# Kernel optimization log

Measured on AMD Instinct MI355X. Metric: run time of the kernel, lower is better.

Reference implementation:

```python
import jax, jax.numpy as jnp
from jax import lax
import numpy as np

TOPK = 100
SCALE = 4.0
EXCEPT_THRESH = 0.01

B, C, H, W = 16, 80, 256, 256


def setup_inputs() -> dict:
    key = jax.random.key(0)
    k1, k2, k3 = jax.random.split(key, 3)
    heatmap = jax.random.uniform(k1, (B, C, H, W), dtype=jnp.float32)
    offset = jax.random.normal(k2, (B, 2, H, W), dtype=jnp.float32)
    wh = jax.random.uniform(k3, (B, 2, H, W), dtype=jnp.float32)
    return {"heatmap": heatmap, "offset": offset, "wh": wh}


def reference(heatmap, offset, wh):
    b, c, h, w = heatmap.shape
    # 3x3 max-pool NMS: keep only local peaks
    pooled = lax.reduce_window(heatmap, -jnp.inf, lax.max,
                               (1, 1, 3, 3), (1, 1, 1, 1), "SAME")
    keep = (pooled == heatmap).astype(heatmap.dtype)
    hm = keep * heatmap
    # top-k over all classes x spatial positions
    flat = hm.reshape(b, -1)                      # [B, C*H*W]
    scores, indices = lax.top_k(flat, TOPK)       # [B, K]
    scores = scores[:, :, None]                   # [B, K, 1]
    ids = (indices // (h * w)).astype(jnp.float32)[:, :, None]
    spatial = indices % (h * w)                   # [B, K] flat spatial index
    topk_ys = (spatial // w).astype(jnp.float32)
    topk_xs = (spatial % w).astype(jnp.float32)
    # gather offset / wh at peak locations
    off = offset.transpose(0, 2, 3, 1).reshape(b, -1, 2)   # [B, H*W, 2]
    whr = wh.transpose(0, 2, 3, 1).reshape(b, -1, 2)       # [B, H*W, 2]
    off_g = jnp.take_along_axis(off, spatial[:, :, None], axis=1)  # [B, K, 2]
    wh_g = jnp.take_along_axis(whr, spatial[:, :, None], axis=1)   # [B, K, 2]
    cx = topk_xs + off_g[:, :, 0]
    cy = topk_ys + off_g[:, :, 1]
    half_w = wh_g[:, :, 0] * 0.5
    half_h = wh_g[:, :, 1] * 0.5
    bboxes = jnp.stack([cx - half_w, cy - half_h, cx + half_w, cy + half_h], axis=-1)  # [B, K, 4]
    # mask out low-score detections with -1
    mask = scores > EXCEPT_THRESH                 # [B, K, 1]
    neg1 = jnp.float32(-1.0)
    ids = jnp.where(mask, ids, neg1)
    scores = jnp.where(mask, scores, neg1)
    bboxes = jnp.where(mask, bboxes, neg1)
    return ids, scores, bboxes * SCALE
```

## Files before the change

kernel.cpp:

```cpp
#include <hip/hip_runtime.h>
#include <stdint.h>

#define HB 16
#define HC 80
#define HH 256
#define HWD 256
#define PLANE (HH * HWD)
#define NPLANES (HB * HC)
#define K_TOP 100
#define CAP 2048
#define CAPR (CAP / 256)
#define OUTCAP 256
#define NEG_INF (-3.402823466e38f)

__device__ __forceinline__ bool better(float a, int ai, float b, int bi) {
    return (a > b) || (a == b && ai < bi);
}

__device__ void bitonic256(float* sv, int* si) {
    int t = threadIdx.x;
    for (unsigned k = 2; k <= 256; k <<= 1) {
        for (unsigned j = k >> 1; j > 0; j >>= 1) {
            __syncthreads();
            unsigned i = (unsigned)t, x = i ^ j;
            if (x > i) {
                float a = sv[i], bv = sv[x];
                int ai = si[i], bi = si[x];
                bool sw = ((i & k) == 0) ? better(bv, bi, a, ai) : better(a, ai, bv, bi);
                if (sw) { sv[i] = bv; si[i] = bi; sv[x] = a; si[x] = ai; }
            }
        }
    }
    __syncthreads();
}

__device__ __forceinline__ float4 loadrow(const float* __restrict__ pl, int r, int lane) {
    int rc = min(max(r, 0), HH - 1);
    float4 v = ((const float4*)(pl + rc * HWD))[lane];
    if (r != rc) { v.x = NEG_INF; v.y = NEG_INF; v.z = NEG_INF; v.w = NEG_INF; }
    return v;
}

__device__ __forceinline__ float4 hmax4(float4 v, int lane) {
    float vl = __shfl_up(v.w, 1);
    float vr = __shfl_down(v.x, 1);
    if (lane == 0) vl = NEG_INF;
    if (lane == 63) vr = NEG_INF;
    float4 h;
    h.x = fmaxf(fmaxf(vl, v.x), v.y);
    h.y = fmaxf(fmaxf(v.x, v.y), v.z);
    h.z = fmaxf(fmaxf(v.y, v.z), v.w);
    h.w = fmaxf(fmaxf(v.z, v.w), vr);
    return h;
}

__global__ __launch_bounds__(256, 4) void k_plane_topk(const float* __restrict__ heat,
                                                       float* __restrict__ wsv,
                                                       int* __restrict__ wsi) {
    int plane = blockIdx.x;
    int c = plane % HC;
    const float* pl = heat + (size_t)plane * PLANE;
    int t = threadIdx.x;
    int lane = t & 63;
    int wid = t >> 6;
    int rs = wid << 6;

    __shared__ float bufv[CAP];
    __shared__ int   bufi[CAP];
    __shared__ float outv[OUTCAP];
    __shared__ int   outi[OUTCAP];
    __shared__ int   cnt, cnt2;
    __shared__ int   sred8[8];
    __shared__ float smax4[4];

    float thr = 0.99f;
    int n = 0;
    for (int attempt = 0; attempt < 3; ++attempt) {
        if (t == 0) cnt = 0;
        __syncthreads();

        float4 rm1 = loadrow(pl, rs - 1, lane);
        float4 r0  = loadrow(pl, rs, lane);
        float4 g0 = loadrow(pl, rs + 1, lane);
        float4 g1 = loadrow(pl, rs + 2, lane);
        float4 g2 = loadrow(pl, rs + 3, lane);
        float4 g3 = loadrow(pl, rs + 4, lane);
        float4 hA = hmax4(rm1, lane);
        float4 hB = hmax4(r0, lane);
        float4 vB = r0;
        int colb = lane << 2;

        for (int i = 0; i < 64; i += 4) {
            float4 m0 = loadrow(pl, rs + i + 5, lane);
            float4 m1 = loadrow(pl, rs + i + 6, lane);
            float4 m2 = loadrow(pl, rs + i + 7, lane);
            float4 m3 = loadrow(pl, rs + i + 8, lane);
#pragma unroll
            for (int u = 0; u < 4; ++u) {
                float4 nr = (u == 0) ? g0 : (u == 1) ? g1 : (u == 2) ? g2 : g3;
                int row = rs + i + u;
                float4 hC = hmax4(nr, lane);
                float p0 = fmaxf(fmaxf(hA.x, hB.x), hC.x);
                float p1 = fmaxf(fmaxf(hA.y, hB.y), hC.y);
                float p2 = fmaxf(fmaxf(hA.z, hB.z), hC.z);
                float p3 = fmaxf(fmaxf(hA.w, hB.w), hC.w);
                if (vB.x >= p0 && vB.x > thr) {
                    int p = atomicAdd(&cnt, 1);
                    if (p < CAP) { bufv[p] = vB.x; bufi[p] = (c << 16) | (row << 8) | colb; }
                }
                if (vB.y >= p1 && vB.y > thr) {
                    int p = atomicAdd(&cnt, 1);
                    if (p < CAP) { bufv[p] = vB.y; bufi[p] = (c << 16) | (row << 8) | (colb + 1); }
                }
                if (vB.z >= p2 && vB.z > thr) {
                    int p = atomicAdd(&cnt, 1);
                    if (p < CAP) { bufv[p] = vB.z; bufi[p] = (c << 16) | (row << 8) | (colb + 2); }
                }
                if (vB.w >= p3 && vB.w > thr) {
                    int p = atomicAdd(&cnt, 1);
                    if (p < CAP) { bufv[p] = vB.w; bufi[p] = (c << 16) | (row << 8) | (colb + 3); }
                }
                hA = hB; hB = hC; vB = nr;
            }
            g0 = m0; g1 = m1; g2 = m2; g3 = m3;
        }
        __syncthreads();
        n = cnt;
        __syncthreads();
        if (n >= K_TOP && n <= CAP) break;
        if (n > CAP) thr = 1.0f - (1.0f - thr) * 0.25f;
        else         thr = 1.0f - (1.0f - thr) * 3.0f;
    }
    int nn = min(n, CAP);

    float regv[CAPR];
#pragma unroll
    for (int k = 0; k < CAPR; ++k) {
        int s = t + (k << 8);
        regv[k] = (s < nn) ? bufv[s] : NEG_INF;
    }

    float T100;
    int par = 0;
    if (nn >= K_TOP) {
        float mx = NEG_INF;
#pragma unroll
        for (int k = 0; k < CAPR; ++k) mx = fmaxf(mx, regv[k]);
        for (int off = 32; off > 0; off >>= 1) mx = fmaxf(mx, __shfl_down(mx, off));
        if (lane == 0) smax4[wid] = mx;
        __syncthreads();
        mx = fmaxf(fmaxf(smax4[0], smax4[1]), fmaxf(smax4[2], smax4[3]));

        unsigned lo = __float_as_uint(thr);
        unsigned hi = __float_as_uint(mx) + 1u;
        while (hi - lo > 1u) {
            unsigned mid = lo + ((hi - lo) >> 1);
            float mv = __uint_as_float(mid);
            int cl = 0;
#pragma unroll
            for (int k = 0; k < CAPR; ++k) cl += (int)__popcll(__ballot(regv[k] >= mv));
            if (lane == 0) sred8[par * 4 + wid] = cl;
            __syncthreads();
            int tot = sred8[par * 4 + 0] + sred8[par * 4 + 1] +
                      sred8[par * 4 + 2] + sred8[par * 4 + 3];
            par ^= 1;
            if (tot >= K_TOP) { lo = mid; if (tot == K_TOP) break; }
            else hi = mid;
        }
        T100 = __uint_as_float(lo);
    } else {
        T100 = NEG_INF;
    }

    outv[t] = NEG_INF; outi[t] = 0x7fffffff;
    if (t == 0) cnt2 = 0;
    __syncthreads();
#pragma unroll
    for (int k = 0; k < CAPR; ++k) {
        int s = t + (k << 8);
        if (s < nn && bufv[s] >= T100) {
            int p = atomicAdd(&cnt2, 1);
            if (p < OUTCAP) { outv[p] = bufv[s]; outi[p] = bufi[s]; }
        }
    }
    __syncthreads();
    int c2 = cnt2;
    if (c2 > K_TOP) bitonic256(outv, outi);
    __syncthreads();
    if (t < K_TOP) {
        wsv[plane * K_TOP + t] = outv[t];
        wsi[plane * K_TOP + t] = outi[t];
    }
}

__global__ __launch_bounds__(256) void k_batch_out(const float* __restrict__ wsv,
                                                   const int* __restrict__ wsi,
                                                   const float* __restrict__ offset,
                                                   const float* __restrict__ wh,
                                                   float* __restrict__ out) {
    int b = blockIdx.x;
    int t = threadIdx.x;
    int lane = t & 63;
    int wid = t >> 6;
    const int NCAND = HC * K_TOP;
    const float* v_in = wsv + b * NCAND;
    const int*   i_in = wsi + b * NCAND;

    __shared__ float outv[OUTCAP];
    __shared__ int   outi[OUTCAP];
    __shared__ int   cnt2;
    __shared__ int   sred8[8];
    __shared__ float sminmax[8];

    float regv[32];
#pragma unroll
    for (int k = 0; k < 32; ++k) {
        int s = t + (k << 8);
        regv[k] = (s < NCAND) ? v_in[s] : NEG_INF;
    }
    int cl0 = 0;
#pragma unroll
    for (int k = 0; k < 32; ++k) cl0 += (int)__popcll(__ballot(regv[k] > NEG_INF));
    if (lane == 0) sred8[wid] = cl0;
    __syncthreads();
    int nreal = sred8[0] + sred8[1] + sred8[2] + sred8[3];
    int par = 1;

    float T100;
    if (nreal >= K_TOP) {
        float mx = NEG_INF, mn = 3.402823466e38f;
#pragma unroll
        for (int k = 0; k < 32; ++k) {
            float v = regv[k];
            if (v > NEG_INF) { mx = fmaxf(mx, v); mn = fminf(mn, v); }
        }
        for (int off = 32; off > 0; off >>= 1) {
            mx = fmaxf(mx, __shfl_down(mx, off));
            mn = fminf(mn, __shfl_down(mn, off));
        }
        if (lane == 0) { sminmax[wid] = mx; sminmax[4 + wid] = mn; }
        __syncthreads();
        mx = fmaxf(fmaxf(sminmax[0], sminmax[1]), fmaxf(sminmax[2], sminmax[3]));
        mn = fminf(fminf(sminmax[4], sminmax[5]), fminf(sminmax[6], sminmax[7]));

        unsigned lo = __float_as_uint(mn);
        unsigned hi = __float_as_uint(mx) + 1u;
        while (hi - lo > 1u) {
            unsigned mid = lo + ((hi - lo) >> 1);
            float mv = __uint_as_float(mid);
            int cl = 0;
#pragma unroll
            for (int k = 0; k < 32; ++k) cl += (int)__popcll(__ballot(regv[k] >= mv));
            if (lane == 0) sred8[par * 4 + wid] = cl;
            __syncthreads();
            int tot = sred8[par * 4 + 0] + sred8[par * 4 + 1] +
                      sred8[par * 4 + 2] + sred8[par * 4 + 3];
            par ^= 1;
            if (tot >= K_TOP) { lo = mid; if (tot == K_TOP) break; }
            else hi = mid;
        }
        T100 = __uint_as_float(lo);
    } else {
        T100 = NEG_INF;
    }

    outv[t] = NEG_INF; outi[t] = 0x7fffffff;
    if (t == 0) cnt2 = 0;
    __syncthreads();
#pragma unroll
    for (int k = 0; k < 32; ++k) {
        int s = t + (k << 8);
        if (s < NCAND && regv[k] >= T100 && regv[k] > NEG_INF) {
            int p = atomicAdd(&cnt2, 1);
            if (p < OUTCAP) { outv[p] = regv[k]; outi[p] = i_in[s]; }
        }
    }
    __syncthreads();
    bitonic256(outv, outi);

    if (t < K_TOP) {
        float val = outv[t];
        int idx = outi[t];
        bool valid = val > 0.01f;
        int cch = idx >> 16;
        int spatial = idx & 0xFFFF;
        int y = spatial >> 8, x = spatial & 0xFF;
        const float* offb = offset + (size_t)b * 2 * PLANE;
        const float* whb  = wh     + (size_t)b * 2 * PLANE;
        float o0 = offb[spatial], o1 = offb[PLANE + spatial];
        float w0 = whb[spatial],  w1 = whb[PLANE + spatial];
        float cx = (float)x + o0, cy = (float)y + o1;
        float hw = w0 * 0.5f, hh = w1 * 0.5f;
        int g = b * K_TOP + t;
        out[g]                = valid ? (float)cch : -1.0f;
        out[HB * K_TOP + g]   = valid ? val        : -1.0f;
        float b0 = valid ? (cx - hw) : -1.0f;
        float b1 = valid ? (cy - hh) : -1.0f;
        float b2 = valid ? (cx + hw) : -1.0f;
        float b3 = valid ? (cy + hh) : -1.0f;
        float* bb = out + 2 * HB * K_TOP + 4 * g;
        bb[0] = b0 * 4.0f; bb[1] = b1 * 4.0f; bb[2] = b2 * 4.0f; bb[3] = b3 * 4.0f;
    }
}

extern "C" void kernel_launch(void* const* d_in, const int* in_sizes, int n_in,
                              void* d_out, int out_size, void* d_ws, size_t ws_size,
                              hipStream_t stream) {
    (void)in_sizes; (void)n_in; (void)out_size; (void)ws_size;
    const float* heat   = (const float*)d_in[0];
    const float* offset = (const float*)d_in[1];
    const float* wh     = (const float*)d_in[2];
    float* out = (float*)d_out;
    float* wsv = (float*)d_ws;
    int*   wsi = (int*)((char*)d_ws + (size_t)NPLANES * K_TOP * sizeof(float));

    k_plane_topk<<<NPLANES, 256, 0, stream>>>(heat, wsv, wsi);
    k_batch_out<<<HB, 256, 0, stream>>>(wsv, wsi, offset, wh, out);
}
```

Before: 484.3 us.

## Widen batch-merge kernel, seed bisection with per-plane thresholds, rank-sort final candidates

The per-plane kernel now writes its 100th-largest threshold to workspace, and skips empty register slots during bisection and compaction. The batch merge kernel moves from 256 to 1024 threads, keeping 8 values per thread instead of 32. It starts the bisection lower bound at the max of the per-plane thresholds, which tightens the search range. The final bitonic sort is replaced by an O(n^2) rank-by-count placement. The aim is to shorten the serial single-block tail kernel, at the cost of more per-iteration reductions across 16 waves.

```diff
diff --git a/kernel.cpp b/kernel.cpp
--- a/kernel.cpp
+++ b/kernel.cpp
@@ -56,7 +56,8 @@
 
 __global__ __launch_bounds__(256, 4) void k_plane_topk(const float* __restrict__ heat,
                                                        float* __restrict__ wsv,
-                                                       int* __restrict__ wsi) {
+                                                       int* __restrict__ wsi,
+                                                       float* __restrict__ wsm) {
     int plane = blockIdx.x;
     int c = plane % HC;
     const float* pl = heat + (size_t)plane * PLANE;
@@ -132,6 +133,7 @@
         else         thr = 1.0f - (1.0f - thr) * 3.0f;
     }
     int nn = min(n, CAP);
+    int kslots = (nn + 255) >> 8;
 
     float regv[CAPR];
 #pragma unroll
@@ -158,7 +160,8 @@
             float mv = __uint_as_float(mid);
             int cl = 0;
 #pragma unroll
-            for (int k = 0; k < CAPR; ++k) cl += (int)__popcll(__ballot(regv[k] >= mv));
+            for (int k = 0; k < CAPR; ++k)
+                if (k < kslots) cl += (int)__popcll(__ballot(regv[k] >= mv));
             if (lane == 0) sred8[par * 4 + wid] = cl;
             __syncthreads();
             int tot = sred8[par * 4 + 0] + sred8[par * 4 + 1] +
@@ -171,16 +174,19 @@
     } else {
         T100 = NEG_INF;
     }
+    if (t == 0) wsm[plane] = T100;
 
     outv[t] = NEG_INF; outi[t] = 0x7fffffff;
     if (t == 0) cnt2 = 0;
     __syncthreads();
 #pragma unroll
     for (int k = 0; k < CAPR; ++k) {
-        int s = t + (k << 8);
-        if (s < nn && bufv[s] >= T100) {
-            int p = atomicAdd(&cnt2, 1);
-            if (p < OUTCAP) { outv[p] = bufv[s]; outi[p] = bufi[s]; }
+        if (k < kslots) {
+            int s = t + (k << 8);
+            if (s < nn && bufv[s] >= T100) {
+                int p = atomicAdd(&cnt2, 1);
+                if (p < OUTCAP) { outv[p] = bufv[s]; outi[p] = bufi[s]; }
+            }
         }
     }
     __syncthreads();
@@ -193,11 +199,12 @@
     }
 }
 
-__global__ __launch_bounds__(256) void k_batch_out(const float* __restrict__ wsv,
-                                                   const int* __restrict__ wsi,
-                                                   const float* __restrict__ offset,
-                                                   const float* __restrict__ wh,
-                                                   float* __restrict__ out) {
+__global__ __launch_bounds__(1024) void k_batch_out(const float* __restrict__ wsv,
+                                                    const int* __restrict__ wsi,
+                                                    const float* __restrict__ wsm,
+                                                    const float* __restrict__ offset,
+                                                    const float* __restrict__ wh,
+                                                    float* __restrict__ out) {
     int b = blockIdx.x;
     int t = threadIdx.x;
     int lane = t & 63;
@@ -208,53 +215,62 @@
 
     __shared__ float outv[OUTCAP];
     __shared__ int   outi[OUTCAP];
+    __shared__ float fv[K_TOP];
+    __shared__ int   fi[K_TOP];
     __shared__ int   cnt2;
-    __shared__ int   sred8[8];
-    __shared__ float sminmax[8];
-
-    float regv[32];
-#pragma unroll
-    for (int k = 0; k < 32; ++k) {
-        int s = t + (k << 8);
+    __shared__ int   sred[32];
+    __shared__ float sr3[48];
+
+    float regv[8];
+#pragma unroll
+    for (int k = 0; k < 8; ++k) {
+        int s = t + (k << 10);
         regv[k] = (s < NCAND) ? v_in[s] : NEG_INF;
     }
+
     int cl0 = 0;
-#pragma unroll
-    for (int k = 0; k < 32; ++k) cl0 += (int)__popcll(__ballot(regv[k] > NEG_INF));
-    if (lane == 0) sred8[wid] = cl0;
-    __syncthreads();
-    int nreal = sred8[0] + sred8[1] + sred8[2] + sred8[3];
+    float mx = NEG_INF, mn = 3.402823466e38f;
+#pragma unroll
+    for (int k = 0; k < 8; ++k) {
+        float v = regv[k];
+        cl0 += (int)__popcll(__ballot(v > NEG_INF));
+        if (v > NEG_INF) { mx = fmaxf(mx, v); mn = fminf(mn, v); }
+    }
+    float wm = (t < HC) ? wsm[b * HC + t] : NEG_INF;
+    for (int off = 32; off > 0; off >>= 1) {
+        mx = fmaxf(mx, __shfl_down(mx, off));
+        mn = fminf(mn, __shfl_down(mn, off));
+        wm = fmaxf(wm, __shfl_down(wm, off));
+    }
+    if (lane == 0) { sred[wid] = cl0; sr3[wid] = mx; sr3[16 + wid] = mn; sr3[32 + wid] = wm; }
+    __syncthreads();
+    int nreal = 0;
+#pragma unroll
+    for (int k = 0; k < 16; ++k) nreal += sred[k];
+    mx = NEG_INF; mn = 3.402823466e38f; wm = NEG_INF;
+#pragma unroll
+    for (int k = 0; k < 16; ++k) {
+        mx = fmaxf(mx, sr3[k]);
+        mn = fminf(mn, sr3[16 + k]);
+        wm = fmaxf(wm, sr3[32 + k]);
+    }
     int par = 1;
 
     float T100;
     if (nreal >= K_TOP) {
-        float mx = NEG_INF, mn = 3.402823466e38f;
-#pragma unroll
-        for (int k = 0; k < 32; ++k) {
-            float v = regv[k];
-            if (v > NEG_INF) { mx = fmaxf(mx, v); mn = fminf(mn, v); }
-        }
-        for (int off = 32; off > 0; off >>= 1) {
-            mx = fmaxf(mx, __shfl_down(mx, off));
-            mn = fminf(mn, __shfl_down(mn, off));
-        }
-        if (lane == 0) { sminmax[wid] = mx; sminmax[4 + wid] = mn; }
-        __syncthreads();
-        mx = fmaxf(fmaxf(sminmax[0], sminmax[1]), fmaxf(sminmax[2], sminmax[3]));
-        mn = fminf(fminf(sminmax[4], sminmax[5]), fminf(sminmax[6], sminmax[7]));
-
-        unsigned lo = __float_as_uint(mn);
+        unsigned lo = __float_as_uint(fmaxf(mn, wm));
         unsigned hi = __float_as_uint(mx) + 1u;
         while (hi - lo > 1u) {
             unsigned mid = lo + ((hi - lo) >> 1);
             float mv = __uint_as_float(mid);
             int cl = 0;
 #pragma unroll
-            for (int k = 0; k < 32; ++k) cl += (int)__popcll(__ballot(regv[k] >= mv));
-            if (lane == 0) sred8[par * 4 + wid] = cl;
+            for (int k = 0; k < 8; ++k) cl += (int)__popcll(__ballot(regv[k] >= mv));
+            if (lane == 0) sred[par * 16 + wid] = cl;
             __syncthreads();
-            int tot = sred8[par * 4 + 0] + sred8[par * 4 + 1] +
-                      sred8[par * 4 + 2] + sred8[par * 4 + 3];
+            int tot = 0;
+#pragma unroll
+            for (int k = 0; k < 16; ++k) tot += sred[par * 16 + k];
             par ^= 1;
             if (tot >= K_TOP) { lo = mid; if (tot == K_TOP) break; }
             else hi = mid;
@@ -264,23 +280,34 @@
         T100 = NEG_INF;
     }
 
-    outv[t] = NEG_INF; outi[t] = 0x7fffffff;
+    if (t < OUTCAP) { outv[t] = NEG_INF; outi[t] = 0x7fffffff; }
+    if (t < K_TOP)  { fv[t] = NEG_INF;   fi[t] = 0x7fffffff; }
     if (t == 0) cnt2 = 0;
     __syncthreads();
 #pragma unroll
-    for (int k = 0; k < 32; ++k) {
-        int s = t + (k << 8);
+    for (int k = 0; k < 8; ++k) {
+        int s = t + (k << 10);
         if (s < NCAND && regv[k] >= T100 && regv[k] > NEG_INF) {
             int p = atomicAdd(&cnt2, 1);
             if (p < OUTCAP) { outv[p] = regv[k]; outi[p] = i_in[s]; }
         }
     }
     __syncthreads();
-    bitonic256(outv, outi);
+
+    int c2m = min(cnt2, OUTCAP);
+    if (t < c2m) {
+        float v = outv[t];
+        int idx = outi[t];
+        int rank = 0;
+        for (int j = 0; j < c2m; ++j)
+            rank += better(outv[j], outi[j], v, idx) ? 1 : 0;
+        if (rank < K_TOP) { fv[rank] = v; fi[rank] = idx; }
+    }
+    __syncthreads();
 
     if (t < K_TOP) {
-        float val = outv[t];
-        int idx = outi[t];
+        float val = fv[t];
+        int idx = fi[t];
         bool valid = val > 0.01f;
         int cch = idx >> 16;
         int spatial = idx & 0xFFFF;
@@ -313,7 +340,8 @@
     float* out = (float*)d_out;
     float* wsv = (float*)d_ws;
     int*   wsi = (int*)((char*)d_ws + (size_t)NPLANES * K_TOP * sizeof(float));
-
-    k_plane_topk<<<NPLANES, 256, 0, stream>>>(heat, wsv, wsi);
-    k_batch_out<<<HB, 256, 0, stream>>>(wsv, wsi, offset, wh, out);
-}
+    float* wsm = (float*)((char*)d_ws + (size_t)NPLANES * K_TOP * 2 * sizeof(float));
+
+    k_plane_topk<<<NPLANES, 256, 0, stream>>>(heat, wsv, wsi, wsm);
+    k_batch_out<<<HB, 1024, 0, stream>>>(wsv, wsi, wsm, offset, wh, out);
+}
```

Measured after the change: 483.0 us, median of 2. About the same (-0.3%).
